# Kernel optimization log

Hardware: AMD Instinct MI355X
Metric: run time of the kernel (lower is better)

The kernel has to match this reference:

```python
import jax, jax.numpy as jnp
import numpy as np

# ---- static config (mirrors PaCoVoxelLoss init) ----
NUM_QUERIES = 20
FACTOR = 64
NUM_GT = 12
K_NEIGHBORS = 8          # repulsion.num_neighbors
REP_EPS = 1e-12          # repulsion.epsilon
BANDWIDTH = 0.03         # repulsion.kernel_bandwidth
RADIUS = 0.07            # repulsion.radius
ALPHA_PARAM = 0.5
BETA_CHAMFER = 20.0
W_CLS, W_REP, W_CH1, W_CH2 = 1.0, 1.0, 1.0, 1.0
PAD_COST = 1e6           # pad value to square the rectangular assignment problem


def _hungarian(cost):
    # Jonker-Volgenant / e-maxx shortest augmenting path; cost: (n, n) float64.
    # Returns col_to_row: for each column j, the row assigned to it.
    n = cost.shape[0]
    INF = 1e18
    u = np.zeros(n + 1); v = np.zeros(n + 1)
    p = np.zeros(n + 1, dtype=np.int64)
    way = np.zeros(n + 1, dtype=np.int64)
    for i in range(1, n + 1):
        p[0] = i; j0 = 0
        minv = np.full(n + 1, INF)
        used = np.zeros(n + 1, dtype=bool)
        while True:
            used[j0] = True
            i0 = p[j0]; delta = INF; j1 = 0
            for j in range(1, n + 1):
                if not used[j]:
                    cur = cost[i0 - 1, j - 1] - u[i0] - v[j]
                    if cur < minv[j]:
                        minv[j] = cur; way[j] = j0
                    if minv[j] < delta:
                        delta = minv[j]; j1 = j
            for j in range(n + 1):
                if used[j]:
                    u[p[j]] += delta; v[j] -= delta
                else:
                    minv[j] -= delta
            j0 = j1
            if p[j0] == 0:
                break
        while j0 != 0:
            j1 = way[j0]; p[j0] = p[j1]; j0 = j1
    return p[1:] - 1


def _match(cost_np):
    # cost_np: (B, Q, P) with P <= Q -> rows (B, P): pred row matched to each gt col.
    Bn, Qn, Pn = cost_np.shape
    rows = np.zeros((Bn, Pn), dtype=np.int64)
    for b in range(Bn):
        sq = np.full((Qn, Qn), PAD_COST, dtype=np.float64)
        sq[:, :Pn] = cost_np[b].astype(np.float64)
        rows[b] = _hungarian(sq)[:Pn]
    return rows


def _gather_q(A, rows):
    # A: (B, Q, P), rows: (B, P) -> A[b, rows[b,p], p] : (B, P)
    return jnp.take_along_axis(A, rows[:, None, :], axis=1)[:, 0, :]


def _bce_logits(x, t):
    return jnp.maximum(x, 0.0) - x * t + jnp.log1p(jnp.exp(-jnp.abs(x)))


def _cost_terms(pred_normals, pred_distances, gt_normals, gt_distances, points, gt_masks):
    mask_f = gt_masks.astype(points.dtype)           # (B, P, N)
    cnt = mask_f.sum(-1)                             # (B, P)
    # |points . n_q - d_q| for all query planes: (B, Q, N)
    pp = jnp.abs(jnp.einsum('bnd,bqd->bqn', points, pred_normals) - pred_distances[:, :, None])
    cham_raw = jnp.einsum('bqn,bpn->bqp', pp, mask_f) / jnp.maximum(cnt, 1.0)[:, None, :]
    has = (cnt > 0)[:, None, :]                      # (B, 1, P)
    normal_sim = 1.0 - jnp.abs(jnp.einsum('bqd,bpd->bqp', pred_normals, gt_normals))
    dist_diff = jnp.abs(pred_distances[:, :, None] - gt_distances[:, None, :])
    cost = normal_sim + 0.5 * dist_diff + 5.0 * jnp.where(has, cham_raw, 1.0)
    return cost, cham_raw, normal_sim, dist_diff, has


def _losses(pred_logits, pred_normals, pred_distances, gt_normals, gt_distances,
            points, reconstructed_points, gt, gt_masks, rows):
    _, cham_raw, normal_sim, dist_diff, has = _cost_terms(
        pred_normals, pred_distances, gt_normals, gt_distances, points, gt_masks)

    # classification loss: target 1 at matched pred rows
    Qn = pred_logits.shape[1]
    cls_target = jax.nn.one_hot(rows, Qn, dtype=pred_logits.dtype).sum(axis=1)  # (B, Q)
    cls_loss = _bce_logits(pred_logits, cls_target).mean()

    # param loss over matched pairs (mean over P matches, mean over B)
    param_loss = (_gather_q(normal_sim, rows).mean(-1) + _gather_q(dist_diff, rows).mean(-1)).mean()

    # pvd chamfer: point-to-plane term, zero for empty masks, /P /B
    pvd_chamfer = _gather_q(jnp.where(has, cham_raw, 0.0), rows).mean()

    # repulsion loss on per-query point groups
    Bn = reconstructed_points.shape[0]
    rp = reconstructed_points.reshape(Bn, NUM_QUERIES, FACTOR, 3)
    d2 = jnp.sum((rp[:, :, :, None, :] - rp[:, :, None, :, :]) ** 2, axis=-1)  # (B,Q,F,F)
    _, idx = jax.lax.top_k(-d2, K_NEIGHBORS)       # k nearest incl. self
    dn = jnp.maximum(jnp.take_along_axis(d2, idx[..., 1:], axis=-1), REP_EPS)  # (B,Q,F,k-1)
    w = jnp.exp(-dn / BANDWIDTH ** 2)
    rep = jnp.maximum(jnp.mean((RADIUS - jnp.sqrt(dn)) * w, axis=(2, 3)), 0.0).mean()

    # fine-grained chamfer (L1 and L2) between reconstructed and gt clouds
    diff = reconstructed_points[:, :, None, :] - gt[:, None, :, :]  # (B, M, G, 3)
    d1 = jnp.abs(diff).sum(-1)
    d2c = (diff ** 2).sum(-1)
    ch1 = (0.5 * (d1.min(axis=2).mean(axis=1) + d1.min(axis=1).mean(axis=1))).mean()
    ch2 = (0.5 * (d2c.min(axis=2).mean(axis=1) + d2c.min(axis=1).mean(axis=1))).mean()

    total = (W_CLS * cls_loss + ALPHA_PARAM * param_loss + BETA_CHAMFER * pvd_chamfer
             + W_REP * rep + W_CH1 * ch1 + W_CH2 * ch2)
    return total


def setup_inputs() -> dict:
    key = jax.random.key(0)
    ks = jax.random.split(key, 10)
    B, Q, P, N, G = 8, NUM_QUERIES, NUM_GT, 4096, 2048

    def unit(k, shape):
        v = jax.random.normal(k, shape, dtype=jnp.float32)
        return v / jnp.linalg.norm(v, axis=-1, keepdims=True)

    return {
        'pred_logits': jax.random.normal(ks[0], (B, Q), dtype=jnp.float32),
        'pred_normals': unit(ks[1], (B, Q, 3)),
        'pred_distances': jax.random.normal(ks[2], (B, Q), dtype=jnp.float32),
        'gt_normals': unit(ks[3], (B, P, 3)),
        'gt_distances': jax.random.normal(ks[4], (B, P), dtype=jnp.float32),
        'gt_masks': jax.random.bernoulli(ks[5], 0.3, (B, P, N)),
        'points': jax.random.normal(ks[6], (B, N, 3), dtype=jnp.float32),
        'reconstructed_points': 0.5 * jax.random.normal(ks[7], (B, Q * FACTOR, 3), dtype=jnp.float32),
        'gt': jax.random.normal(ks[8], (B, G, 3), dtype=jnp.float32),
        'gt_index': jax.random.randint(ks[9], (B, G), 0, P, dtype=jnp.int64) if jax.config.jax_enable_x64 else jax.random.randint(ks[9], (B, G), 0, P, dtype=jnp.int32),
    }


def reference(pred_logits, pred_normals, pred_distances, gt_normals, gt_distances,
              points, reconstructed_points, gt, gt_masks, gt_index):
    cost = _cost_terms(pred_normals, pred_distances, gt_normals, gt_distances, points, gt_masks)[0]
    rows = jnp.asarray(_match(np.asarray(cost)))  # Hungarian (host, like scipy in original)
    return _losses(pred_logits, pred_normals, pred_distances, gt_normals, gt_distances,
                   points, reconstructed_points, gt, gt_masks, rows)
```

## Files before the change

### kernel.cpp

```cpp
#include <hip/hip_runtime.h>
#include <math.h>

#define Bn 8
#define Qn 20
#define Pn 12
#define Nn 4096
#define Gn 2048
#define Mn 1280
#define Fn 64
#define KNB 7
#define SA 8
#define SB 5
#define NPROD 840
#define NFIN 113
#define SCOPE_AGENT __HIP_MEMORY_SCOPE_AGENT


__device__ __forceinline__ float aread(float* p) { return atomicAdd(p, 0.0f); }
__device__ __forceinline__ void ast(float* p, float v) {
    __hip_atomic_store(p, v, __ATOMIC_RELAXED, SCOPE_AGENT);
}
__device__ __forceinline__ float ald(const float* p) {
    return __hip_atomic_load(p, __ATOMIC_RELAXED, SCOPE_AGENT);
}

__device__ __forceinline__ int rdlane_i(int v, int l) {
    return __builtin_amdgcn_readlane(v, l);
}
__device__ __forceinline__ float rdlane_f(float v, int l) {
    return __int_as_float(__builtin_amdgcn_readlane(__float_as_int(v), l));
}
__device__ __forceinline__ unsigned wave_min_u32(unsigned x) {
    unsigned t;
    t = (unsigned)__builtin_amdgcn_update_dpp((int)0xFFFFFFFF, (int)x, 0x111, 0xF, 0xF, false);
    x = t < x ? t : x;
    t = (unsigned)__builtin_amdgcn_update_dpp((int)0xFFFFFFFF, (int)x, 0x112, 0xF, 0xF, false);
    x = t < x ? t : x;
    t = (unsigned)__builtin_amdgcn_update_dpp((int)0xFFFFFFFF, (int)x, 0x114, 0xF, 0xF, false);
    x = t < x ? t : x;
    t = (unsigned)__builtin_amdgcn_update_dpp((int)0xFFFFFFFF, (int)x, 0x118, 0xF, 0xF, false);
    x = t < x ? t : x;
    t = (unsigned)__builtin_amdgcn_update_dpp((int)0xFFFFFFFF, (int)x, 0x142, 0xF, 0xF, false);
    x = t < x ? t : x;
    t = (unsigned)__builtin_amdgcn_update_dpp((int)0xFFFFFFFF, (int)x, 0x143, 0xF, 0xF, false);
    x = t < x ? t : x;
    return x;
}

__device__ __forceinline__ void finpost(float* ws, float* out, unsigned init) {
    unsigned* doneP = (unsigned*)(ws + 7782);
    unsigned* c2P   = (unsigned*)(ws + 7784);
    float* acc = ws + 7776;
    unsigned old = __hip_atomic_fetch_add(c2P, 1u, __ATOMIC_ACQ_REL, SCOPE_AGENT);
    if (old - init == (unsigned)(NFIN - 1)) {
        float a0 = aread(&acc[0]);
        float a1 = aread(&acc[1]);
        float a2 = aread(&acc[2]);
        float a3 = aread(&acc[3]);
        float a4 = aread(&acc[4]);
        float a5 = aread(&acc[5]);
        out[0] = a0 + 0.5f * a1 + 20.f * a2 + a3 + a4 + a5;
        __hip_atomic_store(doneP, init, __ATOMIC_RELAXED, SCOPE_AGENT);
        __hip_atomic_store(c2P,   init, __ATOMIC_RELAXED, SCOPE_AGENT);
    }
}

__global__ void fused_kernel(const float* __restrict__ pred_logits,
                             const float* __restrict__ pred_normals,
                             const float* __restrict__ pred_distances,
                             const float* __restrict__ gt_normals,
                             const float* __restrict__ gt_distances,
                             const float* __restrict__ points,
                             const int*   __restrict__ gt_masks,
                             const float* __restrict__ recon,
                             const float* __restrict__ gt,
                             float* __restrict__ ws,
                             float* __restrict__ out) {
    __shared__ __align__(16) float smem[2 * Pn * 256];
    const int blk = blockIdx.x;
    const int tid = threadIdx.x;

    float* cham = ws;
    float* ns   = ws + 1920;
    float* dd   = ws + 3840;
    float* cost = ws + 5760;
    float* cnt  = ws + 7680;
    float* acc  = ws + 7776;
    unsigned* doneP = (unsigned*)(ws + 7782);
    unsigned* baseP = (unsigned*)(ws + 7783);
    float* rep_part = ws + 7808;
    float* pmA1 = ws + 8192;
    float* pmA2 = ws + 90112;
    float* pmB1 = ws + 172032;
    float* pmB2 = ws + 253952;

    const unsigned init = __hip_atomic_load(baseP, __ATOMIC_RELAXED, SCOPE_AGENT);

    if (blk < 160) {
        if (blk == 0 && tid < 6) ast(&acc[tid], 0.f);
        const int b = blk / Qn, q = blk % Qn;
        const float nx = pred_normals[(b * Qn + q) * 3 + 0];
        const float ny = pred_normals[(b * Qn + q) * 3 + 1];
        const float nz = pred_normals[(b * Qn + q) * 3 + 2];
        const float dq = pred_distances[b * Qn + q];

        float accs[Pn], accw[Pn];
#pragma unroll
        for (int p = 0; p < Pn; ++p) { accs[p] = 0.f; accw[p] = 0.f; }

        const float* ptb = points + (size_t)b * Nn * 3;
        const int*   mb  = gt_masks + (size_t)b * Pn * Nn;

        for (int n = tid; n < Nn; n += 256) {
            float px = ptb[n * 3 + 0], py = ptb[n * 3 + 1], pz = ptb[n * 3 + 2];
            float pp = fabsf(px * nx + py * ny + pz * nz - dq);
#pragma unroll
            for (int p = 0; p < Pn; ++p) {
                float m = (float)mb[(size_t)p * Nn + n];
                accs[p] += pp * m;
                accw[p] += m;
            }
        }
#pragma unroll
        for (int p = 0; p < Pn; ++p) {
            smem[p * 256 + tid] = accs[p];
            smem[(p + Pn) * 256 + tid] = accw[p];
        }
        __syncthreads();
        for (int off = 128; off > 0; off >>= 1) {
            if (tid < off) {
#pragma unroll
                for (int r = 0; r < 2 * Pn; ++r) smem[r * 256 + tid] += smem[r * 256 + tid + off];
            }
            __syncthreads();
        }
        if (tid < Pn) {
            const int p = tid;
            float c  = smem[(p + Pn) * 256];
            float cv = smem[p * 256] / fmaxf(c, 1.f);
            float gnx = gt_normals[(b * Pn + p) * 3 + 0];
            float gny = gt_normals[(b * Pn + p) * 3 + 1];
            float gnz = gt_normals[(b * Pn + p) * 3 + 2];
            float nsim = 1.f - fabsf(nx * gnx + ny * gny + nz * gnz);
            float ddv  = fabsf(dq - gt_distances[b * Pn + p]);
            int idx = (b * Qn + q) * Pn + p;
            ast(&cham[idx], cv);
            ast(&ns[idx],   nsim);
            ast(&dd[idx],   ddv);
            ast(&cost[idx], nsim + 0.5f * ddv + 5.f * ((c > 0.f) ? cv : 1.f));
            if (q == 0) ast(&cnt[b * Pn + p], c);
        }
    } else if (blk < 200) {
        const int wave = tid >> 6, lane = tid & 63;
        const int g = (blk - 160) * 4 + wave;
        float* xs = smem + wave * 192;
        float* ys = xs + 64;
        float* zs = xs + 128;
        const float* base = recon + (size_t)g * Fn * 3;
        xs[lane] = base[lane * 3 + 0];
        ys[lane] = base[lane * 3 + 1];
        zs[lane] = base[lane * 3 + 2];
        float best[KNB];
#pragma unroll
        for (int k = 0; k < KNB; ++k) best[k] = 3.4e38f;
        const float xi = xs[lane], yi = ys[lane], zi = zs[lane];
        for (int j = 0; j < Fn; ++j) {
            float dx = xi - xs[j], dy = yi - ys[j], dz = zi - zs[j];
            float d2 = dx * dx + dy * dy + dz * dz;
            d2 = (j == lane) ? 3.4e38f : d2;
#pragma unroll
            for (int k = 0; k < KNB; ++k) {
                float lo = fminf(best[k], d2);
                float hi = fmaxf(best[k], d2);
                best[k] = lo;
                d2 = hi;
            }
        }
        float sum = 0.f;
#pragma unroll
        for (int k = 0; k < KNB; ++k) {
            float dn = fmaxf(best[k], 1e-12f);
            float w  = expf(-dn / (0.03f * 0.03f));
            sum += (0.07f - sqrtf(dn)) * w;
        }
        for (int off = 32; off > 0; off >>= 1) sum += __shfl_down(sum, off);
        if (lane == 0) ast(&rep_part[g], fmaxf(sum / (float)(Fn * KNB), 0.f));
    } else {
        int cblk = blk - 200;
        float4* tile = reinterpret_cast<float4*>(smem);
        float x, y, z;
        const float* inner;
        float *o1, *o2;
        int idx;
        if (cblk < 40 * SA) {
            int s = cblk % SA, ob = cblk / SA;
            idx = ob * 256 + tid;
            int b = idx / Mn;
            x = recon[idx * 3 + 0]; y = recon[idx * 3 + 1]; z = recon[idx * 3 + 2];
            inner = gt + ((size_t)b * Gn + s * 256) * 3;
            o1 = pmA1 + s * (Bn * Mn); o2 = pmA2 + s * (Bn * Mn);
        } else {
            cblk -= 40 * SA;
            int s = cblk % SB, ob = cblk / SB;
            idx = ob * 256 + tid;
            int b = idx / Gn;
            x = gt[idx * 3 + 0]; y = gt[idx * 3 + 1]; z = gt[idx * 3 + 2];
            inner = recon + ((size_t)b * Mn + s * 256) * 3;
            o1 = pmB1 + s * (Bn * Gn); o2 = pmB2 + s * (Bn * Gn);
        }
        {
            const float* ip = inner + tid * 3;
            float4 tv;
            tv.x = ip[0]; tv.y = ip[1]; tv.z = ip[2]; tv.w = 0.f;
            tile[tid] = tv;
        }
        __syncthreads();
        float m1 = 3.4e38f, m2 = 3.4e38f;
#pragma unroll 4
        for (int j = 0; j < 256; ++j) {
            float4 tv = tile[j];
            float dx = x - tv.x, dy = y - tv.y, dz = z - tv.z;
            float d1 = fabsf(dx) + fabsf(dy) + fabsf(dz);
            float d2 = dx * dx + dy * dy + dz * dz;
            m1 = fminf(m1, d1); m2 = fminf(m2, d2);
        }
        ast(&o1[idx], m1);
        ast(&o2[idx], m2);
    }

    __syncthreads();
    if (tid == 0) __hip_atomic_fetch_add(doneP, 1u, __ATOMIC_RELEASE, SCOPE_AGENT);

    if (blk >= NFIN) return;

    if (tid == 0) {
        while (__hip_atomic_load(doneP, __ATOMIC_RELAXED, SCOPE_AGENT) - init != (unsigned)NPROD)
            __builtin_amdgcn_s_sleep(2);
        (void)__hip_atomic_load(doneP, __ATOMIC_ACQUIRE, SCOPE_AGENT);
    }
    __syncthreads();

    if (blk < 8) {
        if (tid < 64) {
            const int b = blk;
            const int t = tid;
            const int col = t;
            const bool isCol = (col >= 1 && col <= Qn);

            float cr[Pn];
#pragma unroll
            for (int k = 0; k < Pn; ++k) cr[k] = 0.f;
            if (isCol) {
                const float* cb = cost + ((size_t)b * Qn + (col - 1)) * Pn;
#pragma unroll
                for (int k = 0; k < Pn; ++k) cr[k] = ald(&cb[k]);
            }

            float v = 0.f, u = 0.f, minv = 0.f;
            int way = 0, p = 0;

            for (int i = 1; i <= Pn; ++i) {
                minv = 1e30f;
                bool used = false;
                bool rowInPath = false;
                int j0s = 0;
                while (true) {
                    if (col == j0s) used = true;
                    int i0s = (j0s == 0) ? i : rdlane_i(p, j0s);
                    if (t == i0s) rowInPath = true;
                    float u_i0 = rdlane_f(u, i0s);
                    const int bs = i0s - 1;
                    float l10 = (bs & 1) ? cr[1]  : cr[0];
                    float l11 = (bs & 1) ? cr[3]  : cr[2];
                    float l12 = (bs & 1) ? cr[5]  : cr[4];
                    float l13 = (bs & 1) ? cr[7]  : cr[6];
                    float l14 = (bs & 1) ? cr[9]  : cr[8];
                    float l15 = (bs & 1) ? cr[11] : cr[10];
                    float l20 = (bs & 2) ? l11 : l10;
                    float l21 = (bs & 2) ? l13 : l12;
                    float l22 = (bs & 2) ? l15 : l14;
                    float cij = (bs >= 8) ? l22 : ((bs >= 4) ? l21 : l20);
                    if (isCol && !used) {
                        float cur = cij - u_i0 - v;
                        if (cur < minv) { minv = cur; way = j0s; }
                    }
                    float mv = (isCol && !used) ? minv : 1e30f;
                    unsigned kb = __float_as_uint(mv);
                    kb = ((int)kb < 0) ? ~kb : (kb | 0x80000000u);
                    kb = (kb & ~31u) | (unsigned)(col & 31);
                    unsigned kmin = (unsigned)rdlane_i((int)wave_min_u32(kb), 63);
                    int j1 = (int)(kmin & 31u);
                    float delta = rdlane_f(minv, j1);
                    if (used || col == 0) v -= delta;
                    else if (isCol)       minv -= delta;
                    if (rowInPath)        u += delta;
                    j0s = j1;
                    int pj0 = rdlane_i(p, j0s);
                    if (pj0 == 0) break;
                }
                while (j0s != 0) {
                    int wj = rdlane_i(way, j0s);
                    int pw = (wj == 0) ? i : rdlane_i(p, wj);
                    if (col == j0s) p = pw;
                    j0s = wj;
                }
            }

            float cls = 0.f, par = 0.f, pvd = 0.f;
            if (isCol) {
                float x = pred_logits[b * Qn + (col - 1)];
                float tgt = (p > 0) ? 1.f : 0.f;
                cls = fmaxf(x, 0.f) - x * tgt + log1pf(expf(-fabsf(x)));
                if (p > 0) {
                    int idx = (b * Qn + (col - 1)) * Pn + (p - 1);
                    par = ald(&ns[idx]) + ald(&dd[idx]);
                    pvd = (ald(&cnt[b * Pn + (p - 1)]) > 0.f) ? ald(&cham[idx]) : 0.f;
                }
            }
            for (int off = 32; off > 0; off >>= 1) {
                cls += __shfl_down(cls, off);
                par += __shfl_down(par, off);
                pvd += __shfl_down(pvd, off);
            }
            if (t == 0) {
                atomicAdd(&acc[0], cls / (float)(Bn * Qn));
                atomicAdd(&acc[1], par / (float)(Bn * Pn));
                atomicAdd(&acc[2], pvd / (float)(Bn * Pn));
                finpost(ws, out, init);
            }
        }
        return;
    }

    {
        float* s1 = smem;
        float* s2 = smem + 256;
        const int cblk = blk - 8;
        float c1 = 0.f, c2 = 0.f;
        if (cblk < 40) {
            int idx = cblk * 256 + tid;
            float m1 = 3.4e38f, m2 = 3.4e38f;
#pragma unroll
            for (int s = 0; s < SA; ++s) {
                m1 = fminf(m1, ald(&pmA1[s * (Bn * Mn) + idx]));
                m2 = fminf(m2, ald(&pmA2[s * (Bn * Mn) + idx]));
            }
            c1 = m1 * (0.5f / (float)(Bn * Mn));
            c2 = m2 * (0.5f / (float)(Bn * Mn));
        } else if (cblk < 104) {
            int idx = (cblk - 40) * 256 + tid;
            float m1 = 3.4e38f, m2 = 3.4e38f;
#pragma unroll
            for (int s = 0; s < SB; ++s) {
                m1 = fminf(m1, ald(&pmB1[s * (Bn * Gn) + idx]));
                m2 = fminf(m2, ald(&pmB2[s * (Bn * Gn) + idx]));
            }
            c1 = m1 * (0.5f / (float)(Bn * Gn));
            c2 = m2 * (0.5f / (float)(Bn * Gn));
        } else {
            c1 = (tid < Bn * Qn) ? ald(&rep_part[tid]) / (float)(Bn * Qn) : 0.f;
        }
        s1[tid] = c1; s2[tid] = c2;
        __syncthreads();
        for (int off = 128; off > 0; off >>= 1) {
            if (tid < off) { s1[tid] += s1[tid + off]; s2[tid] += s2[tid + off]; }
            __syncthreads();
        }
        if (tid == 0) {
            if (cblk < 104) {
                atomicAdd(&acc[4], s1[0]);
                atomicAdd(&acc[5], s2[0]);
            } else {
                atomicAdd(&acc[3], s1[0]);
            }
            finpost(ws, out, init);
        }
    }
}

extern "C" void kernel_launch(void* const* d_in, const int* in_sizes, int n_in,
                              void* d_out, int out_size, void* d_ws, size_t ws_size,
                              hipStream_t stream) {
    const float* pred_logits    = (const float*)d_in[0];
    const float* pred_normals   = (const float*)d_in[1];
    const float* pred_distances = (const float*)d_in[2];
    const float* gt_normals     = (const float*)d_in[3];
    const float* gt_distances   = (const float*)d_in[4];
    const int*   gt_masks       = (const int*)d_in[5];
    const float* points         = (const float*)d_in[6];
    const float* recon          = (const float*)d_in[7];
    const float* gt             = (const float*)d_in[8];

    fused_kernel<<<NPROD, 256, 0, stream>>>(pred_logits, pred_normals, pred_distances,
                                            gt_normals, gt_distances, points, gt_masks,
                                            recon, gt, (float*)d_ws, (float*)d_out);
}
```

Baseline: 113.2 us.

## Replace grid-wide barrier with per-chunk last-block reductions and fewer chamfer splits

Drops the single global barrier where every producer block waited before finalization. Each chamfer chunk now has its own atomic counter, and the last of its four splits reduces that chunk's minima. Repulsion blocks elect a last finisher to sum their partials, and only the 8 Hungarian blocks wait, and only on the 160 cost blocks. The chamfer inner tiles also grow (512/320 points, 4 splits instead of 8/5), cutting the grid from 840 to 616 blocks. This adds more counters to reset and a wait-for-zero flag so accumulator clearing is ordered before other blocks add to it.

```diff
diff --git a/kernel.cpp b/kernel.cpp
--- a/kernel.cpp
+++ b/kernel.cpp
@@ -9,10 +9,10 @@
 #define Mn 1280
 #define Fn 64
 #define KNB 7
-#define SA 8
-#define SB 5
-#define NPROD 840
-#define NFIN 113
+#define NCOST 160
+#define NREP 40
+#define NBLK 616
+#define C2_TARGET 616
 #define SCOPE_AGENT __HIP_MEMORY_SCOPE_AGENT
 
 
@@ -47,12 +47,17 @@
     return x;
 }
 
-__device__ __forceinline__ void finpost(float* ws, float* out, unsigned init) {
-    unsigned* doneP = (unsigned*)(ws + 7782);
-    unsigned* c2P   = (unsigned*)(ws + 7784);
-    float* acc = ws + 7776;
+__device__ __forceinline__ void wait_zero(float* ws, unsigned init) {
+    unsigned* z = (unsigned*)(ws + 7785);
+    while (__hip_atomic_load(z, __ATOMIC_ACQUIRE, SCOPE_AGENT) - init != 1u)
+        __builtin_amdgcn_s_sleep(1);
+}
+
+__device__ __forceinline__ void bump_c2(float* ws, float* out, unsigned init) {
+    unsigned* c2P = (unsigned*)(ws + 7784);
     unsigned old = __hip_atomic_fetch_add(c2P, 1u, __ATOMIC_ACQ_REL, SCOPE_AGENT);
-    if (old - init == (unsigned)(NFIN - 1)) {
+    if (old - init == (unsigned)(C2_TARGET - 1)) {
+        float* acc = ws + 7776;
         float a0 = aread(&acc[0]);
         float a1 = aread(&acc[1]);
         float a2 = aread(&acc[2]);
@@ -60,8 +65,15 @@
         float a4 = aread(&acc[4]);
         float a5 = aread(&acc[5]);
         out[0] = a0 + 0.5f * a1 + 20.f * a2 + a3 + a4 + a5;
-        __hip_atomic_store(doneP, init, __ATOMIC_RELAXED, SCOPE_AGENT);
-        __hip_atomic_store(c2P,   init, __ATOMIC_RELAXED, SCOPE_AGENT);
+        unsigned* w = (unsigned*)ws;
+        __hip_atomic_store(&w[7782], init, __ATOMIC_RELAXED, SCOPE_AGENT);
+        __hip_atomic_store(&w[7784], init, __ATOMIC_RELAXED, SCOPE_AGENT);
+        __hip_atomic_store(&w[7785], init, __ATOMIC_RELAXED, SCOPE_AGENT);
+        __hip_atomic_store(&w[7786], init, __ATOMIC_RELAXED, SCOPE_AGENT);
+        for (int k = 0; k < 40; ++k)
+            __hip_atomic_store(&w[8040 + k], init, __ATOMIC_RELAXED, SCOPE_AGENT);
+        for (int k = 0; k < 64; ++k)
+            __hip_atomic_store(&w[8080 + k], init, __ATOMIC_RELAXED, SCOPE_AGENT);
     }
 }
 
@@ -77,6 +89,7 @@
                              float* __restrict__ ws,
                              float* __restrict__ out) {
     __shared__ __align__(16) float smem[2 * Pn * 256];
+    __shared__ int sflag;
     const int blk = blockIdx.x;
     const int tid = threadIdx.x;
 
@@ -88,6 +101,9 @@
     float* acc  = ws + 7776;
     unsigned* doneP = (unsigned*)(ws + 7782);
     unsigned* baseP = (unsigned*)(ws + 7783);
+    unsigned* repcP = (unsigned*)(ws + 7786);
+    unsigned* chunkA = (unsigned*)(ws + 8040);
+    unsigned* chunkB = (unsigned*)(ws + 8080);
     float* rep_part = ws + 7808;
     float* pmA1 = ws + 8192;
     float* pmA2 = ws + 90112;
@@ -96,7 +112,7 @@
 
     const unsigned init = __hip_atomic_load(baseP, __ATOMIC_RELAXED, SCOPE_AGENT);
 
-    if (blk < 160) {
+    if (blk < NCOST) {
         if (blk == 0 && tid < 6) ast(&acc[tid], 0.f);
         const int b = blk / Qn, q = blk % Qn;
         const float nx = pred_normals[(b * Qn + q) * 3 + 0];
@@ -150,99 +166,29 @@
             ast(&cost[idx], nsim + 0.5f * ddv + 5.f * ((c > 0.f) ? cv : 1.f));
             if (q == 0) ast(&cnt[b * Pn + p], c);
         }
-    } else if (blk < 200) {
-        const int wave = tid >> 6, lane = tid & 63;
-        const int g = (blk - 160) * 4 + wave;
-        float* xs = smem + wave * 192;
-        float* ys = xs + 64;
-        float* zs = xs + 128;
-        const float* base = recon + (size_t)g * Fn * 3;
-        xs[lane] = base[lane * 3 + 0];
-        ys[lane] = base[lane * 3 + 1];
-        zs[lane] = base[lane * 3 + 2];
-        float best[KNB];
-#pragma unroll
-        for (int k = 0; k < KNB; ++k) best[k] = 3.4e38f;
-        const float xi = xs[lane], yi = ys[lane], zi = zs[lane];
-        for (int j = 0; j < Fn; ++j) {
-            float dx = xi - xs[j], dy = yi - ys[j], dz = zi - zs[j];
-            float d2 = dx * dx + dy * dy + dz * dz;
-            d2 = (j == lane) ? 3.4e38f : d2;
-#pragma unroll
-            for (int k = 0; k < KNB; ++k) {
-                float lo = fminf(best[k], d2);
-                float hi = fmaxf(best[k], d2);
-                best[k] = lo;
-                d2 = hi;
-            }
-        }
-        float sum = 0.f;
-#pragma unroll
-        for (int k = 0; k < KNB; ++k) {
-            float dn = fmaxf(best[k], 1e-12f);
-            float w  = expf(-dn / (0.03f * 0.03f));
-            sum += (0.07f - sqrtf(dn)) * w;
-        }
-        for (int off = 32; off > 0; off >>= 1) sum += __shfl_down(sum, off);
-        if (lane == 0) ast(&rep_part[g], fmaxf(sum / (float)(Fn * KNB), 0.f));
-    } else {
-        int cblk = blk - 200;
-        float4* tile = reinterpret_cast<float4*>(smem);
-        float x, y, z;
-        const float* inner;
-        float *o1, *o2;
-        int idx;
-        if (cblk < 40 * SA) {
-            int s = cblk % SA, ob = cblk / SA;
-            idx = ob * 256 + tid;
-            int b = idx / Mn;
-            x = recon[idx * 3 + 0]; y = recon[idx * 3 + 1]; z = recon[idx * 3 + 2];
-            inner = gt + ((size_t)b * Gn + s * 256) * 3;
-            o1 = pmA1 + s * (Bn * Mn); o2 = pmA2 + s * (Bn * Mn);
-        } else {
-            cblk -= 40 * SA;
-            int s = cblk % SB, ob = cblk / SB;
-            idx = ob * 256 + tid;
-            int b = idx / Gn;
-            x = gt[idx * 3 + 0]; y = gt[idx * 3 + 1]; z = gt[idx * 3 + 2];
-            inner = recon + ((size_t)b * Mn + s * 256) * 3;
-            o1 = pmB1 + s * (Bn * Gn); o2 = pmB2 + s * (Bn * Gn);
-        }
-        {
-            const float* ip = inner + tid * 3;
-            float4 tv;
-            tv.x = ip[0]; tv.y = ip[1]; tv.z = ip[2]; tv.w = 0.f;
-            tile[tid] = tv;
-        }
-        __syncthreads();
-        float m1 = 3.4e38f, m2 = 3.4e38f;
-#pragma unroll 4
-        for (int j = 0; j < 256; ++j) {
-            float4 tv = tile[j];
-            float dx = x - tv.x, dy = y - tv.y, dz = z - tv.z;
-            float d1 = fabsf(dx) + fabsf(dy) + fabsf(dz);
-            float d2 = dx * dx + dy * dy + dz * dz;
-            m1 = fminf(m1, d1); m2 = fminf(m2, d2);
-        }
-        ast(&o1[idx], m1);
-        ast(&o2[idx], m2);
-    }
-
-    __syncthreads();
-    if (tid == 0) __hip_atomic_fetch_add(doneP, 1u, __ATOMIC_RELEASE, SCOPE_AGENT);
-
-    if (blk >= NFIN) return;
-
-    if (tid == 0) {
-        while (__hip_atomic_load(doneP, __ATOMIC_RELAXED, SCOPE_AGENT) - init != (unsigned)NPROD)
-            __builtin_amdgcn_s_sleep(2);
-        (void)__hip_atomic_load(doneP, __ATOMIC_ACQUIRE, SCOPE_AGENT);
-    }
-    __syncthreads();
-
-    if (blk < 8) {
+        __syncthreads();
+        if (tid == 0) {
+            if (blk == 0) {
+                unsigned* z = (unsigned*)(ws + 7785);
+                __hip_atomic_store(z, init + 1u, __ATOMIC_RELEASE, SCOPE_AGENT);
+            }
+            __hip_atomic_fetch_add(doneP, 1u, __ATOMIC_RELEASE, SCOPE_AGENT);
+        }
+
+        if (blk >= 8) {
+            if (tid == 0) bump_c2(ws, out, init);
+            return;
+        }
+
+        if (tid == 0) {
+            while (__hip_atomic_load(doneP, __ATOMIC_RELAXED, SCOPE_AGENT) - init != (unsigned)NCOST)
+                __builtin_amdgcn_s_sleep(2);
+            (void)__hip_atomic_load(doneP, __ATOMIC_ACQUIRE, SCOPE_AGENT);
+        }
+        __syncthreads();
+
         if (tid < 64) {
-            const int b = blk;
+            const int b2 = blk;
             const int t = tid;
             const int col = t;
             const bool isCol = (col >= 1 && col <= Qn);
@@ -251,7 +197,7 @@
 #pragma unroll
             for (int k = 0; k < Pn; ++k) cr[k] = 0.f;
             if (isCol) {
-                const float* cb = cost + ((size_t)b * Qn + (col - 1)) * Pn;
+                const float* cb = cost + ((size_t)b2 * Qn + (col - 1)) * Pn;
 #pragma unroll
                 for (int k = 0; k < Pn; ++k) cr[k] = ald(&cb[k]);
             }
@@ -308,13 +254,13 @@
 
             float cls = 0.f, par = 0.f, pvd = 0.f;
             if (isCol) {
-                float x = pred_logits[b * Qn + (col - 1)];
+                float x = pred_logits[b2 * Qn + (col - 1)];
                 float tgt = (p > 0) ? 1.f : 0.f;
                 cls = fmaxf(x, 0.f) - x * tgt + log1pf(expf(-fabsf(x)));
                 if (p > 0) {
-                    int idx = (b * Qn + (col - 1)) * Pn + (p - 1);
+                    int idx = (b2 * Qn + (col - 1)) * Pn + (p - 1);
                     par = ald(&ns[idx]) + ald(&dd[idx]);
-                    pvd = (ald(&cnt[b * Pn + (p - 1)]) > 0.f) ? ald(&cham[idx]) : 0.f;
+                    pvd = (ald(&cnt[b2 * Pn + (p - 1)]) > 0.f) ? ald(&cham[idx]) : 0.f;
                 }
             }
             for (int off = 32; off > 0; off >>= 1) {
@@ -326,56 +272,168 @@
                 atomicAdd(&acc[0], cls / (float)(Bn * Qn));
                 atomicAdd(&acc[1], par / (float)(Bn * Pn));
                 atomicAdd(&acc[2], pvd / (float)(Bn * Pn));
-                finpost(ws, out, init);
-            }
-        }
+                bump_c2(ws, out, init);
+            }
+        }
+        return;
+    } else if (blk < 200) {
+        const int wave = tid >> 6, lane = tid & 63;
+        const int g = (blk - NCOST) * 4 + wave;
+        float* xs = smem + wave * 192;
+        float* ys = xs + 64;
+        float* zs = xs + 128;
+        const float* base = recon + (size_t)g * Fn * 3;
+        xs[lane] = base[lane * 3 + 0];
+        ys[lane] = base[lane * 3 + 1];
+        zs[lane] = base[lane * 3 + 2];
+        float best[KNB];
+#pragma unroll
+        for (int k = 0; k < KNB; ++k) best[k] = 3.4e38f;
+        const float xi = xs[lane], yi = ys[lane], zi = zs[lane];
+        for (int j = 0; j < Fn; ++j) {
+            float dx = xi - xs[j], dy = yi - ys[j], dz = zi - zs[j];
+            float d2 = dx * dx + dy * dy + dz * dz;
+            d2 = (j == lane) ? 3.4e38f : d2;
+#pragma unroll
+            for (int k = 0; k < KNB; ++k) {
+                float lo = fminf(best[k], d2);
+                float hi = fmaxf(best[k], d2);
+                best[k] = lo;
+                d2 = hi;
+            }
+        }
+        float sum = 0.f;
+#pragma unroll
+        for (int k = 0; k < KNB; ++k) {
+            float dn = fmaxf(best[k], 1e-12f);
+            float w  = expf(-dn / (0.03f * 0.03f));
+            sum += (0.07f - sqrtf(dn)) * w;
+        }
+        for (int off = 32; off > 0; off >>= 1) sum += __shfl_down(sum, off);
+        if (lane == 0) ast(&rep_part[g], fmaxf(sum / (float)(Fn * KNB), 0.f));
+        __syncthreads();
+        if (tid == 0) {
+            unsigned old = __hip_atomic_fetch_add(repcP, 1u, __ATOMIC_ACQ_REL, SCOPE_AGENT);
+            sflag = (old - init == (unsigned)(NREP - 1)) ? 1 : 0;
+        }
+        __syncthreads();
+        if (sflag) {
+            float* s1 = smem + 768;
+            float c1 = (tid < Bn * Qn) ? ald(&rep_part[tid]) / (float)(Bn * Qn) : 0.f;
+            s1[tid] = c1;
+            __syncthreads();
+            for (int off = 128; off > 0; off >>= 1) {
+                if (tid < off) s1[tid] += s1[tid + off];
+                __syncthreads();
+            }
+            if (tid == 0) {
+                wait_zero(ws, init);
+                atomicAdd(&acc[3], s1[0]);
+            }
+        }
+        if (tid == 0) bump_c2(ws, out, init);
         return;
     }
 
-    {
+    float4* tile = reinterpret_cast<float4*>(smem);
+    float* o1;
+    float* o2;
+    unsigned* ctr;
+    int idx, chunk, s, nslots;
+    float scale;
+    float m1 = 3.4e38f, m2 = 3.4e38f;
+
+    if (blk < 360) {
+        int a = blk - 200;
+        chunk = a >> 2; s = a & 3;
+        idx = chunk * 256 + tid;
+        const int b = chunk / 5;
+        const float* ip = gt + ((size_t)b * Gn + s * 512) * 3;
+        {
+            float4 tv;
+            int j0 = tid;
+            tv.x = ip[j0 * 3 + 0]; tv.y = ip[j0 * 3 + 1]; tv.z = ip[j0 * 3 + 2]; tv.w = 0.f;
+            tile[j0] = tv;
+            int j1 = tid + 256;
+            tv.x = ip[j1 * 3 + 0]; tv.y = ip[j1 * 3 + 1]; tv.z = ip[j1 * 3 + 2]; tv.w = 0.f;
+            tile[j1] = tv;
+        }
+        __syncthreads();
+        const float x = recon[idx * 3 + 0], y = recon[idx * 3 + 1], z = recon[idx * 3 + 2];
+#pragma unroll 4
+        for (int j = 0; j < 512; ++j) {
+            float4 tv = tile[j];
+            float dx = x - tv.x, dy = y - tv.y, dz = z - tv.z;
+            float d1 = fabsf(dx) + fabsf(dy) + fabsf(dz);
+            float d2 = dx * dx + dy * dy + dz * dz;
+            m1 = fminf(m1, d1); m2 = fminf(m2, d2);
+        }
+        o1 = pmA1; o2 = pmA2; ctr = &chunkA[chunk];
+        nslots = Bn * Mn; scale = 0.5f / (float)(Bn * Mn);
+    } else {
+        int a = blk - 360;
+        chunk = a >> 2; s = a & 3;
+        idx = chunk * 256 + tid;
+        const int b = chunk / 8;
+        const float* ip = recon + ((size_t)b * Mn + s * 320) * 3;
+        {
+            float4 tv;
+            int j0 = tid;
+            if (j0 < 320) {
+                tv.x = ip[j0 * 3 + 0]; tv.y = ip[j0 * 3 + 1]; tv.z = ip[j0 * 3 + 2]; tv.w = 0.f;
+                tile[j0] = tv;
+            }
+            int j1 = tid + 256;
+            if (j1 < 320) {
+                tv.x = ip[j1 * 3 + 0]; tv.y = ip[j1 * 3 + 1]; tv.z = ip[j1 * 3 + 2]; tv.w = 0.f;
+                tile[j1] = tv;
+            }
+        }
+        __syncthreads();
+        const float x = gt[idx * 3 + 0], y = gt[idx * 3 + 1], z = gt[idx * 3 + 2];
+#pragma unroll 4
+        for (int j = 0; j < 320; ++j) {
+            float4 tv = tile[j];
+            float dx = x - tv.x, dy = y - tv.y, dz = z - tv.z;
+            float d1 = fabsf(dx) + fabsf(dy) + fabsf(dz);
+            float d2 = dx * dx + dy * dy + dz * dz;
+            m1 = fminf(m1, d1); m2 = fminf(m2, d2);
+        }
+        o1 = pmB1; o2 = pmB2; ctr = &chunkB[chunk];
+        nslots = Bn * Gn; scale = 0.5f / (float)(Bn * Gn);
+    }
+
+    ast(&o1[s * nslots + idx], m1);
+    ast(&o2[s * nslots + idx], m2);
+    __syncthreads();
+    if (tid == 0) {
+        unsigned old = __hip_atomic_fetch_add(ctr, 1u, __ATOMIC_ACQ_REL, SCOPE_AGENT);
+        sflag = (old - init == 3u) ? 1 : 0;
+    }
+    __syncthreads();
+    if (sflag) {
+        float m1c = 3.4e38f, m2c = 3.4e38f;
+#pragma unroll
+        for (int ss = 0; ss < 4; ++ss) {
+            m1c = fminf(m1c, ald(&o1[ss * nslots + idx]));
+            m2c = fminf(m2c, ald(&o2[ss * nslots + idx]));
+        }
         float* s1 = smem;
         float* s2 = smem + 256;
-        const int cblk = blk - 8;
-        float c1 = 0.f, c2 = 0.f;
-        if (cblk < 40) {
-            int idx = cblk * 256 + tid;
-            float m1 = 3.4e38f, m2 = 3.4e38f;
-#pragma unroll
-            for (int s = 0; s < SA; ++s) {
-                m1 = fminf(m1, ald(&pmA1[s * (Bn * Mn) + idx]));
-                m2 = fminf(m2, ald(&pmA2[s * (Bn * Mn) + idx]));
-            }
-            c1 = m1 * (0.5f / (float)(Bn * Mn));
-            c2 = m2 * (0.5f / (float)(Bn * Mn));
-        } else if (cblk < 104) {
-            int idx = (cblk - 40) * 256 + tid;
-            float m1 = 3.4e38f, m2 = 3.4e38f;
-#pragma unroll
-            for (int s = 0; s < SB; ++s) {
-                m1 = fminf(m1, ald(&pmB1[s * (Bn * Gn) + idx]));
-                m2 = fminf(m2, ald(&pmB2[s * (Bn * Gn) + idx]));
-            }
-            c1 = m1 * (0.5f / (float)(Bn * Gn));
-            c2 = m2 * (0.5f / (float)(Bn * Gn));
-        } else {
-            c1 = (tid < Bn * Qn) ? ald(&rep_part[tid]) / (float)(Bn * Qn) : 0.f;
-        }
-        s1[tid] = c1; s2[tid] = c2;
+        s1[tid] = m1c * scale;
+        s2[tid] = m2c * scale;
         __syncthreads();
         for (int off = 128; off > 0; off >>= 1) {
             if (tid < off) { s1[tid] += s1[tid + off]; s2[tid] += s2[tid + off]; }
             __syncthreads();
         }
         if (tid == 0) {
-            if (cblk < 104) {
-                atomicAdd(&acc[4], s1[0]);
-                atomicAdd(&acc[5], s2[0]);
-            } else {
-                atomicAdd(&acc[3], s1[0]);
-            }
-            finpost(ws, out, init);
+            wait_zero(ws, init);
+            atomicAdd(&acc[4], s1[0]);
+            atomicAdd(&acc[5], s2[0]);
         }
     }
+    if (tid == 0) bump_c2(ws, out, init);
 }
 
 extern "C" void kernel_launch(void* const* d_in, const int* in_sizes, int n_in,
@@ -391,7 +449,7 @@
     const float* recon          = (const float*)d_in[7];
     const float* gt             = (const float*)d_in[8];
 
-    fused_kernel<<<NPROD, 256, 0, stream>>>(pred_logits, pred_normals, pred_distances,
-                                            gt_normals, gt_distances, points, gt_masks,
-                                            recon, gt, (float*)d_ws, (float*)d_out);
-}
+    fused_kernel<<<NBLK, 256, 0, stream>>>(pred_logits, pred_normals, pred_distances,
+                                           gt_normals, gt_distances, points, gt_masks,
+                                           recon, gt, (float*)d_ws, (float*)d_out);
+}
```

Measured after the change: 130.3 us. +15.1%, slower.
